# Optimization experiments

Measured on AMD Instinct MI355X. Metric: run time of the kernel, lower is better.

## Reference

```python
import jax, jax.numpy as jnp
import numpy as np
from jax import lax

C = 32           # cell_state_size (channels, depthwise groups)
B = 4            # batch
D = H = W = 64   # lattice dims
STEPS = 8        # propagation depth


def setup_inputs() -> dict:
    key = jax.random.key(0)
    k1, k2 = jax.random.split(key)
    cube_states = jax.random.normal(k1, (B, C, D, H, W), dtype=jnp.float32)
    # torch depthwise Conv3d weight: [C_out, C_in/groups=1, 3, 3, 3]
    weight = jax.random.normal(k2, (C, 1, 3, 3, 3), dtype=jnp.float32) * 0.1
    return {"cube_states": cube_states, "weight": weight, "depth": STEPS}


def _depthwise_conv3d(x, w):
    # x: [B, C, D, H, W], w: [C, 1, 3, 3, 3] -> depthwise via feature_group_count=C
    return lax.conv_general_dilated(
        x, w,
        window_strides=(1, 1, 1),
        padding=((1, 1), (1, 1), (1, 1)),
        dimension_numbers=("NCDHW", "OIDHW", "NCDHW"),
        feature_group_count=C,
    )


def reference(cube_states, weight, depth):
    x = cube_states
    for _ in range(depth):
        residual = _depthwise_conv3d(x, weight)
        x = jax.nn.gelu(x + residual, approximate=False)  # torch nn.GELU() is exact (erf)
    return x
```

## Files before the change

kernel.cpp:

```cpp
#include <hip/hip_runtime.h>
#include <math.h>

#define Bn 4
#define Cn 32
#define Dn 64
#define Hn 64
#define Wn 64
#define PLANE (Hn * Wn)
#define DT 16
#define HT 32
#define LSTRIDE 68
#define LROWS (HT + 2)
#define LPLANE (LROWS * LSTRIDE)

__device__ __forceinline__ float gelu_exact(float x) {
    float s = fabsf(x) * 0.70710678118654752f;
    float t = __builtin_amdgcn_rcpf(fmaf(0.3275911f, s, 1.0f));
    float P = t * fmaf(t, fmaf(t, fmaf(t, fmaf(t, 1.061405429f, -1.453152027f),
                                       1.421413741f), -0.284496736f), 0.254829592f);
    float E = __builtin_amdgcn_exp2f(-s * s * 1.4426950408889634f);
    float q = P * E;
    float hxq = 0.5f * x * q;
    return x > 0.f ? x - hxq : hxq;
}

__device__ __forceinline__ void read_row(const float* base, float f[10]) {
    float4 a = *(const float4*)(base);
    float4 b = *(const float4*)(base + 4);
    float2 c = *(const float2*)(base + 8);
    f[0] = a.x; f[1] = a.y; f[2] = a.z; f[3] = a.w;
    f[4] = b.x; f[5] = b.y; f[6] = b.z; f[7] = b.w;
    f[8] = c.x; f[9] = c.y;
}

__device__ __forceinline__ void acc_row(const float f[10], float w0t, float w1t,
                                        float w2t, float acc[8]) {
#pragma unroll
    for (int j = 0; j < 8; j++) {
        acc[j] = fmaf(f[j],     w0t, acc[j]);
        acc[j] = fmaf(f[j + 1], w1t, acc[j]);
        acc[j] = fmaf(f[j + 2], w2t, acc[j]);
    }
}

__global__ __launch_bounds__(256, 4)
void EmergentSpatialPropagation_step(const float* __restrict__ src,
                                     const float* __restrict__ wgt,
                                     float* __restrict__ dst) {
    __shared__ __align__(16) float lds[4 * LPLANE];

    const int tid  = threadIdx.x;
    const int dblk = blockIdx.x >> 1;
    const int hblk = blockIdx.x & 1;
    const int d0   = dblk * DT;
    const int h0   = hblk * HT;
    const int c    = blockIdx.y;
    const int b    = blockIdx.z;
    const size_t base = ((size_t)(b * Cn + c)) * (size_t)(Dn * PLANE);

    for (int i = tid; i < 4 * LPLANE; i += 256) lds[i] = 0.0f;

    float wt[27];
#pragma unroll
    for (int k = 0; k < 27; k++) wt[k] = wgt[c * 27 + k];

    const int h  = tid >> 3;
    const int w0 = (tid & 7) << 3;
    const int m  = tid & 15;

    auto slot = [&](int p) -> float* { return &lds[((p + 1) & 3) * LPLANE]; };

    auto load_g = [&](int p, float4 G[2], float4& GH) {
        GH = make_float4(0.f, 0.f, 0.f, 0.f);
        if ((unsigned)p < (unsigned)Dn) {
            const float4* g = (const float4*)(src + base + (size_t)p * PLANE);
            G[0] = g[h0 * 16 + tid];
            G[1] = g[h0 * 16 + 256 + tid];
            if (tid < 32) {
                int row = (tid < 16) ? (h0 - 1) : (h0 + HT);
                if ((unsigned)row < (unsigned)Hn) GH = g[row * 16 + (tid & 15)];
            }
        } else {
            G[0] = make_float4(0.f, 0.f, 0.f, 0.f);
            G[1] = make_float4(0.f, 0.f, 0.f, 0.f);
        }
    };

    auto write_plane = [&](int p, const float4 G[2], float4 GH) {
        float* pl = slot(p);
#pragma unroll
        for (int i = 0; i < 2; i++) {
            int idx = i * 256 + tid;
            int row = (idx >> 4) + 1;
            float prev = __shfl_up(G[i].w, 1);
            if (m == 0) prev = 0.f;
            float4 Wv = make_float4(prev, G[i].x, G[i].y, G[i].z);
            *(float4*)(pl + row * LSTRIDE + 4 * m) = Wv;
            if (m == 15) pl[row * LSTRIDE + 64] = G[i].w;
        }
        if (tid < 32) {
            int prow = (tid < 16) ? 0 : (LROWS - 1);
            float prev = __shfl_up(GH.w, 1);
            if (m == 0) prev = 0.f;
            float4 Wv = make_float4(prev, GH.x, GH.y, GH.z);
            *(float4*)(pl + prow * LSTRIDE + 4 * m) = Wv;
            if (m == 15) pl[prow * LSTRIDE + 64] = GH.w;
        }
    };

    __syncthreads();
    {
        float4 Ga[2], Gb[2], Gc[2], Ha, Hb, Hc;
        load_g(d0 - 1, Ga, Ha); load_g(d0, Gb, Hb); load_g(d0 + 1, Gc, Hc);
        write_plane(d0 - 1, Ga, Ha); write_plane(d0, Gb, Hb); write_plane(d0 + 1, Gc, Hc);
    }
    __syncthreads();

    float C0[3][10], C1[3][10];
#pragma unroll
    for (int ky = 0; ky < 3; ky++)
        read_row(slot(d0) + (h + ky) * LSTRIDE + w0, C0[ky]);

    for (int it = 0; it < DT; it++) {
        const int dz = d0 + it;

        float4 G[2], GH;
        if (it < DT - 1) load_g(dz + 2, G, GH);

#pragma unroll
        for (int ky = 0; ky < 3; ky++)
            read_row(slot(dz + 1) + (h + ky) * LSTRIDE + w0, C1[ky]);

        float acc[8] = {0, 0, 0, 0, 0, 0, 0, 0};

#pragma unroll
        for (int ky = 0; ky < 3; ky++) {
            float T[10];
            read_row(slot(dz - 1) + (h + ky) * LSTRIDE + w0, T);
            acc_row(T, wt[ky * 3 + 0], wt[ky * 3 + 1], wt[ky * 3 + 2], acc);
        }
#pragma unroll
        for (int ky = 0; ky < 3; ky++)
            acc_row(C0[ky], wt[9 + ky * 3 + 0], wt[9 + ky * 3 + 1], wt[9 + ky * 3 + 2], acc);
#pragma unroll
        for (int ky = 0; ky < 3; ky++)
            acc_row(C1[ky], wt[18 + ky * 3 + 0], wt[18 + ky * 3 + 1], wt[18 + ky * 3 + 2], acc);

        float* dptr = dst + base + (size_t)dz * PLANE + (h0 + h) * Wn + w0;
        float4 o0 = make_float4(gelu_exact(C0[1][1] + acc[0]),
                                gelu_exact(C0[1][2] + acc[1]),
                                gelu_exact(C0[1][3] + acc[2]),
                                gelu_exact(C0[1][4] + acc[3]));
        float4 o1 = make_float4(gelu_exact(C0[1][5] + acc[4]),
                                gelu_exact(C0[1][6] + acc[5]),
                                gelu_exact(C0[1][7] + acc[6]),
                                gelu_exact(C0[1][8] + acc[7]));
        *(float4*)(dptr)     = o0;
        *(float4*)(dptr + 4) = o1;

        if (it < DT - 1) {
            write_plane(dz + 2, G, GH);
            __syncthreads();
        }

#pragma unroll
        for (int ky = 0; ky < 3; ky++)
#pragma unroll
            for (int k = 0; k < 10; k++) C0[ky][k] = C1[ky][k];
    }
}

extern "C" void kernel_launch(void* const* d_in, const int* in_sizes, int n_in,
                              void* d_out, int out_size, void* d_ws, size_t ws_size,
                              hipStream_t stream) {
    const float* x   = (const float*)d_in[0];
    const float* wgt = (const float*)d_in[1];
    float* out = (float*)d_out;
    float* ws  = (float*)d_ws;

    dim3 grid((Dn / DT) * 2, Cn, Bn);
    dim3 block(256);

    const float* src = x;
    for (int s = 0; s < 8; s++) {
        float* dst = (s & 1) ? out : ws;
        EmergentSpatialPropagation_step<<<grid, block, 0, stream>>>(src, wgt, dst);
        src = dst;
    }
}
```

Before: 798.8 us.

## Stream depth planes once with rolling accumulators and double-buffered LDS

Each LDS plane is now read once per thread and scattered into three rolling depth accumulators (A0/A1/A2), replacing three per-plane row reads and the carried C0/C1 register copies. LDS shrinks from four planes to two (double buffer), and the depth tile is halved from 16 to 8, doubling the block count. The aim is less LDS traffic and register pressure plus higher occupancy and parallelism. The cost is more halo plane reloads per block and one extra pipeline warm-up iteration for every output tile.

Result: faster. 644.6 us (-19.3%).

```diff
diff --git a/kernel.cpp b/kernel.cpp
--- a/kernel.cpp
+++ b/kernel.cpp
@@ -7,7 +7,7 @@
 #define Hn 64
 #define Wn 64
 #define PLANE (Hn * Wn)
-#define DT 16
+#define DT 8
 #define HT 32
 #define LSTRIDE 68
 #define LROWS (HT + 2)
@@ -47,7 +47,7 @@
 void EmergentSpatialPropagation_step(const float* __restrict__ src,
                                      const float* __restrict__ wgt,
                                      float* __restrict__ dst) {
-    __shared__ __align__(16) float lds[4 * LPLANE];
+    __shared__ __align__(16) float lds[2 * LPLANE];
 
     const int tid  = threadIdx.x;
     const int dblk = blockIdx.x >> 1;
@@ -58,7 +58,7 @@
     const int b    = blockIdx.z;
     const size_t base = ((size_t)(b * Cn + c)) * (size_t)(Dn * PLANE);
 
-    for (int i = tid; i < 4 * LPLANE; i += 256) lds[i] = 0.0f;
+    for (int i = tid; i < 2 * LPLANE; i += 256) lds[i] = 0.0f;
 
     float wt[27];
 #pragma unroll
@@ -68,7 +68,7 @@
     const int w0 = (tid & 7) << 3;
     const int m  = tid & 15;
 
-    auto slot = [&](int p) -> float* { return &lds[((p + 1) & 3) * LPLANE]; };
+    auto sl = [&](int p) -> float* { return &lds[((p - d0 + 1) & 1) * LPLANE]; };
 
     auto load_g = [&](int p, float4 G[2], float4& GH) {
         GH = make_float4(0.f, 0.f, 0.f, 0.f);
@@ -86,8 +86,7 @@
         }
     };
 
-    auto write_plane = [&](int p, const float4 G[2], float4 GH) {
-        float* pl = slot(p);
+    auto write_plane = [&](float* pl, const float4 G[2], float4 GH) {
 #pragma unroll
         for (int i = 0; i < 2; i++) {
             int idx = i * 256 + tid;
@@ -110,63 +109,63 @@
 
     __syncthreads();
     {
-        float4 Ga[2], Gb[2], Gc[2], Ha, Hb, Hc;
-        load_g(d0 - 1, Ga, Ha); load_g(d0, Gb, Hb); load_g(d0 + 1, Gc, Hc);
-        write_plane(d0 - 1, Ga, Ha); write_plane(d0, Gb, Hb); write_plane(d0 + 1, Gc, Hc);
+        float4 Ga[2], Ha;
+        load_g(d0 - 1, Ga, Ha);
+        write_plane(sl(d0 - 1), Ga, Ha);
     }
     __syncthreads();
 
-    float C0[3][10], C1[3][10];
+    float A0[8], A1[8], A2[8], prevc[8];
 #pragma unroll
-    for (int ky = 0; ky < 3; ky++)
-        read_row(slot(d0) + (h + ky) * LSTRIDE + w0, C0[ky]);
+    for (int j = 0; j < 8; j++) { A0[j] = 0.f; A1[j] = 0.f; A2[j] = 0.f; prevc[j] = 0.f; }
 
-    for (int it = 0; it < DT; it++) {
-        const int dz = d0 + it;
+#pragma unroll 1
+    for (int jj = 0; jj <= DT + 1; jj++) {
+        const int p = d0 - 1 + jj;
+        const bool do_stage = (jj <= DT);
 
         float4 G[2], GH;
-        if (it < DT - 1) load_g(dz + 2, G, GH);
+        if (do_stage) load_g(p + 1, G, GH);
 
-#pragma unroll
-        for (int ky = 0; ky < 3; ky++)
-            read_row(slot(dz + 1) + (h + ky) * LSTRIDE + w0, C1[ky]);
+        float fm[10], fc[10], fq[10];
+        const float* pl = sl(p);
+        read_row(pl + (h + 0) * LSTRIDE + w0, fm);
+        read_row(pl + (h + 1) * LSTRIDE + w0, fc);
+        read_row(pl + (h + 2) * LSTRIDE + w0, fq);
 
-        float acc[8] = {0, 0, 0, 0, 0, 0, 0, 0};
+        acc_row(fm, wt[0],  wt[1],  wt[2],  A2);
+        acc_row(fc, wt[3],  wt[4],  wt[5],  A2);
+        acc_row(fq, wt[6],  wt[7],  wt[8],  A2);
+        acc_row(fm, wt[9],  wt[10], wt[11], A1);
+        acc_row(fc, wt[12], wt[13], wt[14], A1);
+        acc_row(fq, wt[15], wt[16], wt[17], A1);
+        acc_row(fm, wt[18], wt[19], wt[20], A0);
+        acc_row(fc, wt[21], wt[22], wt[23], A0);
+        acc_row(fq, wt[24], wt[25], wt[26], A0);
 
-#pragma unroll
-        for (int ky = 0; ky < 3; ky++) {
-            float T[10];
-            read_row(slot(dz - 1) + (h + ky) * LSTRIDE + w0, T);
-            acc_row(T, wt[ky * 3 + 0], wt[ky * 3 + 1], wt[ky * 3 + 2], acc);
-        }
-#pragma unroll
-        for (int ky = 0; ky < 3; ky++)
-            acc_row(C0[ky], wt[9 + ky * 3 + 0], wt[9 + ky * 3 + 1], wt[9 + ky * 3 + 2], acc);
-#pragma unroll
-        for (int ky = 0; ky < 3; ky++)
-            acc_row(C1[ky], wt[18 + ky * 3 + 0], wt[18 + ky * 3 + 1], wt[18 + ky * 3 + 2], acc);
-
-        float* dptr = dst + base + (size_t)dz * PLANE + (h0 + h) * Wn + w0;
-        float4 o0 = make_float4(gelu_exact(C0[1][1] + acc[0]),
-                                gelu_exact(C0[1][2] + acc[1]),
-                                gelu_exact(C0[1][3] + acc[2]),
-                                gelu_exact(C0[1][4] + acc[3]));
-        float4 o1 = make_float4(gelu_exact(C0[1][5] + acc[4]),
-                                gelu_exact(C0[1][6] + acc[5]),
-                                gelu_exact(C0[1][7] + acc[6]),
-                                gelu_exact(C0[1][8] + acc[7]));
-        *(float4*)(dptr)     = o0;
-        *(float4*)(dptr + 4) = o1;
-
-        if (it < DT - 1) {
-            write_plane(dz + 2, G, GH);
-            __syncthreads();
+        if (jj >= 2) {
+            float* dp = dst + base + (size_t)(p - 1) * PLANE + (h0 + h) * Wn + w0;
+            float4 o0 = make_float4(gelu_exact(prevc[0] + A0[0]),
+                                    gelu_exact(prevc[1] + A0[1]),
+                                    gelu_exact(prevc[2] + A0[2]),
+                                    gelu_exact(prevc[3] + A0[3]));
+            float4 o1 = make_float4(gelu_exact(prevc[4] + A0[4]),
+                                    gelu_exact(prevc[5] + A0[5]),
+                                    gelu_exact(prevc[6] + A0[6]),
+                                    gelu_exact(prevc[7] + A0[7]));
+            *(float4*)(dp)     = o0;
+            *(float4*)(dp + 4) = o1;
         }
 
 #pragma unroll
-        for (int ky = 0; ky < 3; ky++)
+        for (int j = 0; j < 8; j++) { A0[j] = A1[j]; A1[j] = A2[j]; A2[j] = 0.f; }
 #pragma unroll
-            for (int k = 0; k < 10; k++) C0[ky][k] = C1[ky][k];
+        for (int j = 0; j < 8; j++) prevc[j] = fc[j + 1];
+
+        if (do_stage) {
+            write_plane(sl(p + 1), G, GH);
+            __syncthreads();
+        }
     }
 }
 
```
